# Kernel optimization log

Measured on AMD Instinct MI355X. Metric: run time of the kernel, lower is better.

Reference implementation:

```python
import jax, jax.numpy as jnp
import numpy as np

ATT_PROP = 2  # config['att_prop']
NEG_BIAS = 1e23


def _bucket(d):
    # standard coref-style distance bucketing into 10 buckets
    d = jnp.abs(d)
    return jnp.where(d <= 4, d,
           jnp.where(d <= 7, 5,
           jnp.where(d <= 15, 6,
           jnp.where(d <= 31, 7,
           jnp.where(d <= 63, 8, 9))))).astype(jnp.int32)


def setup_inputs() -> dict:
    key = jax.random.key(0)
    ks = jax.random.split(key, 12)
    B, N, M, D, H = 2, 1024, 2048, 512, 64
    scale = 0.02  # init_weights_std

    update = jax.random.normal(ks[0], (B, N, D), jnp.float32)
    span_begin = jnp.sort(jax.random.randint(ks[1], (B, N), 0, 2000), axis=-1).astype(jnp.int32)
    span_end = (span_begin + jax.random.randint(ks[2], (B, N), 0, 10)).astype(jnp.int32)
    square_mask = jnp.ones((B, N, N), jnp.float32)
    cand_span_vecs = jax.random.normal(ks[3], (B, M, D), jnp.float32)
    # unique prune indices per batch (a pruned span maps to one candidate slot)
    prune_indices_hoi = jnp.stack([
        jnp.sort(jax.random.permutation(jax.random.fold_in(ks[4], b), M)[:N])
        for b in range(B)]).astype(jnp.int32)
    span_lengths = jnp.array([900, 1024], dtype=jnp.int32)

    W_left = jax.random.normal(ks[5], (D, H), jnp.float32) * scale
    W_right = jax.random.normal(ks[6], (D, H), jnp.float32) * scale
    b_h = jnp.zeros((H,), jnp.float32)
    dist_emb = jax.random.normal(ks[7], (10, H), jnp.float32) * scale
    v_out = jax.random.normal(ks[8], (H,), jnp.float32) * scale
    b_out = jnp.zeros((), jnp.float32)
    W_gate = jax.random.normal(ks[9], (2 * D, D), jnp.float32) * scale
    b_gate = jnp.zeros((D,), jnp.float32)

    return dict(update=update, square_mask=square_mask, cand_span_vecs=cand_span_vecs,
                span_begin=span_begin, span_end=span_end,
                prune_indices_hoi=prune_indices_hoi, span_lengths=span_lengths,
                W_left=W_left, W_right=W_right, b_h=b_h, dist_emb=dist_emb,
                v_out=v_out, b_out=b_out, W_gate=W_gate, b_gate=b_gate)


def reference(update, square_mask, cand_span_vecs, span_begin, span_end,
              prune_indices_hoi, span_lengths, W_left, W_right, b_h,
              dist_emb, v_out, b_out, W_gate, b_gate):
    B, N, D = update.shape
    # pairwise distance features are iteration-invariant: precompute once
    dist = dist_emb[_bucket(span_begin[:, :, None] - span_begin[:, None, :])]  # [B,N,N,H]
    bias = -(1.0 - square_mask) * NEG_BIAS  # [B,N,N]

    for _ in range(ATT_PROP):
        left = update @ W_left    # [B,N,H]
        right = update @ W_right  # [B,N,H]
        h = jax.nn.relu(left[:, :, None, :] + right[:, None, :, :] + dist + b_h)  # [B,N,N,H]
        scores = jnp.einsum('bijh,h->bij', h, v_out) + b_out  # [B,N,N]
        probs = jax.nn.softmax(scores + bias, axis=-1)
        ctxt = jnp.einsum('bij,bjd->bid', probs, update)  # [B,N,D]
        g = jax.nn.sigmoid(jnp.concatenate([update, ctxt], axis=-1) @ W_gate + b_gate)
        update = g * update + (1.0 - g) * ctxt

    # overwrite_spans_hoi: scatter first span_lengths[b] updated vectors back
    valid = jnp.arange(N) < span_lengths[:, None]  # [B,N]

    def scatter_one(cand, idx, upd, m):
        cur = cand[idx]  # [N,D]
        vals = jnp.where(m[:, None], upd, cur)  # invalid rows write back original
        return cand.at[idx].set(vals)

    cand_new = jax.vmap(scatter_one)(cand_span_vecs, prune_indices_hoi, update, valid)
    return cand_new, update
```

## Files before the change

kernel.cpp:

```cpp
#include <hip/hip_runtime.h>
#include <cstdint>

#define NB 2
#define NN 1024
#define MM 2048
#define DD 512
#define HH 64
#define IT 16
#define JT 64
#define ST 68

typedef __attribute__((ext_vector_type(8))) short bf16x8;
typedef __attribute__((ext_vector_type(4))) float f32x4;

__device__ inline ushort f2bf(float x) {
  union { float f; uint32_t u; } v; v.f = x;
  uint32_t u = v.u;
  u += 0x7FFF + ((u >> 16) & 1);
  return (ushort)(u >> 16);
}

#define GLDS(gp, lp) \
  __builtin_amdgcn_global_load_lds( \
      (const __attribute__((address_space(1))) void*)(gp), \
      (__attribute__((address_space(3))) void*)(lp), 16, 0, 0)

__global__ __launch_bounds__(256) void lr_kernel(
    const float* __restrict__ U, const float* __restrict__ Wl,
    const float* __restrict__ Wr, float* __restrict__ left,
    float* __restrict__ right) {
  __shared__ float u[8][DD];
  const int block = blockIdx.x;
  const int tid = threadIdx.x;
  const float4* Uv = (const float4*)(U + (size_t)block * 8 * DD);
  float4* uv = (float4*)&u[0][0];
#pragma unroll
  for (int t = 0; t < 4; ++t) uv[tid + t * 256] = Uv[tid + t * 256];
  __syncthreads();
  const int h = tid & 63;
  const int isR = (tid >> 6) & 1;
  const int rbase = tid >> 7;
  const float* __restrict__ W = isR ? Wr : Wl;
  float acc[4] = {0.f, 0.f, 0.f, 0.f};
  for (int k0 = 0; k0 < DD; k0 += 4) {
    float w0 = W[(k0 + 0) * HH + h];
    float w1 = W[(k0 + 1) * HH + h];
    float w2 = W[(k0 + 2) * HH + h];
    float w3 = W[(k0 + 3) * HH + h];
#pragma unroll
    for (int r = 0; r < 4; ++r) {
      float4 u4 = *(const float4*)&u[rbase + r * 2][k0];
      acc[r] = fmaf(u4.w, w3, fmaf(u4.z, w2, fmaf(u4.y, w1, fmaf(u4.x, w0, acc[r]))));
    }
  }
  float* out = isR ? right : left;
#pragma unroll
  for (int r = 0; r < 4; ++r)
    out[(size_t)(block * 8 + rbase + r * 2) * HH + h] = acc[r];
}

__global__ __launch_bounds__(256) void conv_t(
    const float* __restrict__ in, ushort* __restrict__ out_row,
    ushort* __restrict__ out_T, int R, int C, int write_row) {
  __shared__ float tile[64][65];
  const int b = blockIdx.z;
  const int r0 = blockIdx.y * 64, c0 = blockIdx.x * 64;
  const int tx = threadIdx.x & 15, ty = threadIdx.x >> 4;
  const float* inb = in + (size_t)b * R * C;
#pragma unroll
  for (int p = 0; p < 4; ++p) {
    const int r = ty + p * 16;
    const float4 v = *(const float4*)&inb[(size_t)(r0 + r) * C + c0 + tx * 4];
    tile[r][tx * 4 + 0] = v.x; tile[r][tx * 4 + 1] = v.y;
    tile[r][tx * 4 + 2] = v.z; tile[r][tx * 4 + 3] = v.w;
    if (write_row) {
      ushort4 o = make_ushort4(f2bf(v.x), f2bf(v.y), f2bf(v.z), f2bf(v.w));
      *(ushort4*)&out_row[(size_t)b * R * C + (size_t)(r0 + r) * C + c0 + tx * 4] = o;
    }
  }
  __syncthreads();
  ushort* oT = out_T + (size_t)b * R * C;
#pragma unroll
  for (int p = 0; p < 4; ++p) {
    const int rr = ty + p * 16;
    ushort4 o;
    o.x = f2bf(tile[tx * 4 + 0][rr]);
    o.y = f2bf(tile[tx * 4 + 1][rr]);
    o.z = f2bf(tile[tx * 4 + 2][rr]);
    o.w = f2bf(tile[tx * 4 + 3][rr]);
    *(ushort4*)&oT[(size_t)(c0 + rr) * R + r0 + tx * 4] = o;
  }
}

__global__ __launch_bounds__(256) void score_compute(
    const float* __restrict__ left, const float* __restrict__ right,
    const int* __restrict__ span_begin, const float* __restrict__ mask,
    const float* __restrict__ dist_emb, const float* __restrict__ b_h,
    const float* __restrict__ v_out, float* __restrict__ scores) {
  __shared__ float Rt[JT][ST];
  __shared__ float LDb[IT * 10][ST];
  __shared__ float Lt[IT][ST];
  __shared__ float Dbh[10][ST];
  __shared__ float Vl[ST];
  __shared__ int sbi[IT];
  __shared__ int sbj[JT];
  const int b = blockIdx.z;
  const int i0 = blockIdx.y * IT;
  const int j0 = blockIdx.x * JT;
  const int tid = threadIdx.x;

  for (int f = tid; f < JT * 16; f += 256) {
    int r = f >> 4, h4 = f & 15;
    *(float4*)&Rt[r][h4 * 4] =
        *(const float4*)&right[((size_t)b * NN + j0 + r) * HH + h4 * 4];
  }
  {
    int r = tid >> 4, h4 = tid & 15;
    *(float4*)&Lt[r][h4 * 4] =
        *(const float4*)&left[((size_t)b * NN + i0 + r) * HH + h4 * 4];
  }
  for (int f = tid; f < 160; f += 256) {
    int bk = f >> 4, h4 = f & 15;
    float4 d = *(const float4*)&dist_emb[bk * HH + h4 * 4];
    float4 bh = *(const float4*)&b_h[h4 * 4];
    d.x += bh.x; d.y += bh.y; d.z += bh.z; d.w += bh.w;
    *(float4*)&Dbh[bk][h4 * 4] = d;
  }
  if (tid < 16) *(float4*)&Vl[tid * 4] = *(const float4*)&v_out[tid * 4];
  if (tid >= 64 && tid < 64 + IT) sbi[tid - 64] = span_begin[b * NN + i0 + tid - 64];
  if (tid >= 128 && tid < 128 + JT) sbj[tid - 128] = span_begin[b * NN + j0 + tid - 128];
  __syncthreads();
  {
    const int i = tid >> 4, h4 = tid & 15;
    const float4 l4 = *(const float4*)&Lt[i][h4 * 4];
#pragma unroll
    for (int bk = 0; bk < 10; ++bk) {
      float4 d = *(const float4*)&Dbh[bk][h4 * 4];
      d.x += l4.x; d.y += l4.y; d.z += l4.z; d.w += l4.w;
      *(float4*)&LDb[i * 10 + bk][h4 * 4] = d;
    }
  }
  __syncthreads();

  const int i = tid >> 4, jq = tid & 15;
  const float* LDbF = &LDb[0][0];
  const int my_sbi = sbi[i];
  int rowL[4];
#pragma unroll
  for (int jj = 0; jj < 4; ++jj) {
    const int jl = jq * 4 + jj;
    int d = sbj[jl] - my_sbi;
    d = d < 0 ? -d : d;
    const int bk =
        d <= 4 ? d : (d <= 7 ? 5 : (d <= 15 ? 6 : (d <= 31 ? 7 : (d <= 63 ? 8 : 9))));
    rowL[jj] = (i * 10 + bk) * ST;
  }
  float acc[4] = {0.f, 0.f, 0.f, 0.f};
#pragma unroll
  for (int hq = 0; hq < 16; ++hq) {
    const float4 v4 = *(const float4*)&Vl[hq * 4];
#pragma unroll
    for (int jj = 0; jj < 4; ++jj) {
      const float4 z = *(const float4*)&LDbF[rowL[jj] + hq * 4];
      const float4 r4 = *(const float4*)&Rt[jq * 4 + jj][hq * 4];
      float x0 = fmaxf(z.x + r4.x, 0.f);
      float x1 = fmaxf(z.y + r4.y, 0.f);
      float x2 = fmaxf(z.z + r4.z, 0.f);
      float x3 = fmaxf(z.w + r4.w, 0.f);
      acc[jj] = fmaf(x0, v4.x, acc[jj]);
      acc[jj] = fmaf(x1, v4.y, acc[jj]);
      acc[jj] = fmaf(x2, v4.z, acc[jj]);
      acc[jj] = fmaf(x3, v4.w, acc[jj]);
    }
  }
  const size_t rowoff = ((size_t)b * NN + i0 + i) * NN + j0 + jq * 4;
  const float4 m4 = *(const float4*)&mask[rowoff];
  float4 s4;
  s4.x = acc[0] - (1.0f - m4.x) * 1e23f;
  s4.y = acc[1] - (1.0f - m4.y) * 1e23f;
  s4.z = acc[2] - (1.0f - m4.z) * 1e23f;
  s4.w = acc[3] - (1.0f - m4.w) * 1e23f;
  *(float4*)&scores[rowoff] = s4;
}

__global__ __launch_bounds__(256) void softmax_bf(
    const float* __restrict__ scores, ushort* __restrict__ pbf) {
  const int wave = threadIdx.x >> 6, lane = threadIdx.x & 63;
  const int row = blockIdx.x * 4 + wave;
  const float4* p = (const float4*)(scores + (size_t)row * NN);
  float4 v[4];
  float mx = -3.0e38f;
#pragma unroll
  for (int q = 0; q < 4; ++q) {
    v[q] = p[lane + q * 64];
    mx = fmaxf(mx, fmaxf(fmaxf(v[q].x, v[q].y), fmaxf(v[q].z, v[q].w)));
  }
#pragma unroll
  for (int off = 32; off; off >>= 1) mx = fmaxf(mx, __shfl_xor(mx, off));
  float sum = 0.f;
#pragma unroll
  for (int q = 0; q < 4; ++q) {
    v[q].x = __expf(v[q].x - mx); v[q].y = __expf(v[q].y - mx);
    v[q].z = __expf(v[q].z - mx); v[q].w = __expf(v[q].w - mx);
    sum += v[q].x + v[q].y + v[q].z + v[q].w;
  }
#pragma unroll
  for (int off = 32; off; off >>= 1) sum += __shfl_xor(sum, off);
  const float inv = 1.0f / sum;
  ushort4* ob = (ushort4*)(pbf + (size_t)row * NN);
#pragma unroll
  for (int q = 0; q < 4; ++q) {
    ushort4 o = make_ushort4(f2bf(v[q].x * inv), f2bf(v[q].y * inv),
                             f2bf(v[q].z * inv), f2bf(v[q].w * inv));
    ob[lane + q * 64] = o;
  }
}

__global__ __launch_bounds__(256) void gemm_ctxt_mfma(
    const ushort* __restrict__ Pbf, const ushort* __restrict__ UT,
    float* __restrict__ Cf, ushort* __restrict__ Cbf) {
  __shared__ ushort As[64 * 64];
  __shared__ ushort Bs[64 * 64];
  const int b = blockIdx.z;
  const int m0 = blockIdx.y * 64, n0 = blockIdx.x * 64;
  const int tid = threadIdx.x;
  const int lane = tid & 63, wave = tid >> 6;
  const int wm = (wave >> 1) * 32, wn = (wave & 1) * 32;
  const ushort* Ab = Pbf + (size_t)b * NN * NN;
  const ushort* Bb = UT + (size_t)b * DD * NN;
  f32x4 acc[2][2] = {};
  const int fm = lane & 15, quad = lane >> 4;
  for (int k0 = 0; k0 < NN; k0 += 64) {
#pragma unroll
    for (int t = 0; t < 2; ++t) {
      const int idx = tid + t * 256;
      const int r = idx >> 3, c8 = idx & 7;
      const int g = c8 ^ (r & 7);
      GLDS(Ab + (size_t)(m0 + r) * NN + k0 + g * 8, As + idx * 8);
      GLDS(Bb + (size_t)(n0 + r) * NN + k0 + g * 8, Bs + idx * 8);
    }
    __syncthreads();
#pragma unroll
    for (int s = 0; s < 2; ++s) {
      bf16x8 af[2], bfr[2];
#pragma unroll
      for (int tm = 0; tm < 2; ++tm) {
        const int row = wm + tm * 16 + fm;
        const int c8 = (s * 4 + quad) ^ (row & 7);
        af[tm] = *(const bf16x8*)&As[row * 64 + c8 * 8];
      }
#pragma unroll
      for (int tn = 0; tn < 2; ++tn) {
        const int row = wn + tn * 16 + fm;
        const int c8 = (s * 4 + quad) ^ (row & 7);
        bfr[tn] = *(const bf16x8*)&Bs[row * 64 + c8 * 8];
      }
#pragma unroll
      for (int tm = 0; tm < 2; ++tm)
#pragma unroll
        for (int tn = 0; tn < 2; ++tn)
          acc[tm][tn] = __builtin_amdgcn_mfma_f32_16x16x32_bf16(
              af[tm], bfr[tn], acc[tm][tn], 0, 0, 0);
    }
    __syncthreads();
  }
#pragma unroll
  for (int tm = 0; tm < 2; ++tm)
#pragma unroll
    for (int tn = 0; tn < 2; ++tn) {
      const int col = n0 + wn + tn * 16 + fm;
#pragma unroll
      for (int r = 0; r < 4; ++r) {
        const int row = m0 + wm + tm * 16 + quad * 4 + r;
        const float vv = acc[tm][tn][r];
        const size_t off = (size_t)b * NN * DD + (size_t)row * DD + col;
        Cf[off] = vv;
        Cbf[off] = f2bf(vv);
      }
    }
}

__global__ __launch_bounds__(256) void gemm_gate_mfma(
    const ushort* __restrict__ Ubf, const ushort* __restrict__ Cbf,
    const ushort* __restrict__ WgT, const float* __restrict__ bg,
    const float* __restrict__ Uf, const float* __restrict__ Cf,
    float* __restrict__ Uout) {
  __shared__ ushort As[64 * 64];
  __shared__ ushort Bs[64 * 64];
  const int b = blockIdx.z;
  const int m0 = blockIdx.y * 64, n0 = blockIdx.x * 64;
  const int tid = threadIdx.x;
  const int lane = tid & 63, wave = tid >> 6;
  const int wm = (wave >> 1) * 32, wn = (wave & 1) * 32;
  f32x4 acc[2][2] = {};
  const int fm = lane & 15, quad = lane >> 4;
  for (int k0 = 0; k0 < 2 * DD; k0 += 64) {
    const ushort* Abase = (k0 < DD) ? (Ubf + (size_t)b * NN * DD)
                                    : (Cbf + (size_t)b * NN * DD);
    const int kc = k0 & (DD - 1);
#pragma unroll
    for (int t = 0; t < 2; ++t) {
      const int idx = tid + t * 256;
      const int r = idx >> 3, c8 = idx & 7;
      const int g = c8 ^ (r & 7);
      GLDS(Abase + (size_t)(m0 + r) * DD + kc + g * 8, As + idx * 8);
      GLDS(WgT + (size_t)(n0 + r) * (2 * DD) + k0 + g * 8, Bs + idx * 8);
    }
    __syncthreads();
#pragma unroll
    for (int s = 0; s < 2; ++s) {
      bf16x8 af[2], bfr[2];
#pragma unroll
      for (int tm = 0; tm < 2; ++tm) {
        const int row = wm + tm * 16 + fm;
        const int c8 = (s * 4 + quad) ^ (row & 7);
        af[tm] = *(const bf16x8*)&As[row * 64 + c8 * 8];
      }
#pragma unroll
      for (int tn = 0; tn < 2; ++tn) {
        const int row = wn + tn * 16 + fm;
        const int c8 = (s * 4 + quad) ^ (row & 7);
        bfr[tn] = *(const bf16x8*)&Bs[row * 64 + c8 * 8];
      }
#pragma unroll
      for (int tm = 0; tm < 2; ++tm)
#pragma unroll
        for (int tn = 0; tn < 2; ++tn)
          acc[tm][tn] = __builtin_amdgcn_mfma_f32_16x16x32_bf16(
              af[tm], bfr[tn], acc[tm][tn], 0, 0, 0);
    }
    __syncthreads();
  }
#pragma unroll
  for (int tm = 0; tm < 2; ++tm)
#pragma unroll
    for (int tn = 0; tn < 2; ++tn) {
      const int col = n0 + wn + tn * 16 + fm;
      const float bgv = bg[col];
#pragma unroll
      for (int r = 0; r < 4; ++r) {
        const int row = m0 + wm + tm * 16 + quad * 4 + r;
        const size_t off = (size_t)b * NN * DD + (size_t)row * DD + col;
        const float g = 1.f / (1.f + __expf(-(acc[tm][tn][r] + bgv)));
        Uout[off] = g * Uf[off] + (1.f - g) * Cf[off];
      }
    }
}

__global__ __launch_bounds__(256) void out_copy(
    const float* __restrict__ cand, const float* __restrict__ upd,
    float* __restrict__ out) {
  const int t = blockIdx.x * 256 + threadIdx.x;
  float4* o4 = (float4*)out;
  if (t < 524288) o4[t] = ((const float4*)cand)[t];
  else o4[t] = ((const float4*)upd)[t - 524288];
}

__global__ __launch_bounds__(128) void scatter_k(
    float* __restrict__ out_cand, const float* __restrict__ upd,
    const int* __restrict__ prune, const int* __restrict__ span_len) {
  const int row = blockIdx.x;
  const int b = row >> 10, i = row & 1023;
  if (i >= span_len[b]) return;
  const int dst = prune[row];
  const float4* src = (const float4*)(upd + (size_t)row * DD);
  float4* d = (float4*)(out_cand + ((size_t)b * MM + dst) * DD);
  d[threadIdx.x] = src[threadIdx.x];
}

extern "C" void kernel_launch(void* const* d_in, const int* in_sizes, int n_in,
                              void* d_out, int out_size, void* d_ws, size_t ws_size,
                              hipStream_t stream) {
  const float* update = (const float*)d_in[0];
  const float* mask = (const float*)d_in[1];
  const float* cand = (const float*)d_in[2];
  const int* span_begin = (const int*)d_in[3];
  const int* prune = (const int*)d_in[5];
  const int* span_len = (const int*)d_in[6];
  const float* Wl = (const float*)d_in[7];
  const float* Wr = (const float*)d_in[8];
  const float* b_h = (const float*)d_in[9];
  const float* dist_emb = (const float*)d_in[10];
  const float* v_out = (const float*)d_in[11];
  const float* Wg = (const float*)d_in[13];
  const float* b_gate = (const float*)d_in[14];

  char* w = (char*)d_ws;
  float* left = (float*)w;      w += (size_t)NB * NN * HH * 4;
  float* right = (float*)w;     w += (size_t)NB * NN * HH * 4;
  float* scores = (float*)w;    w += (size_t)NB * NN * NN * 4;
  ushort* probs_bf = (ushort*)w; w += (size_t)NB * NN * NN * 2;
  float* ctxt_f = (float*)w;    w += (size_t)NB * NN * DD * 4;
  ushort* ctxt_bf = (ushort*)w; w += (size_t)NB * NN * DD * 2;
  float* upd1 = (float*)w;      w += (size_t)NB * NN * DD * 4;
  float* upd2 = (float*)w;      w += (size_t)NB * NN * DD * 4;
  ushort* Ubf = (ushort*)w;     w += (size_t)NB * NN * DD * 2;
  ushort* UT = (ushort*)w;      w += (size_t)NB * NN * DD * 2;
  ushort* WgT = (ushort*)w;     w += (size_t)2 * DD * DD * 2;

  float* out = (float*)d_out;

  conv_t<<<dim3(8, 16, 1), 256, 0, stream>>>(Wg, WgT, WgT, 2 * DD, DD, 0);

  const float* Ucur = update;
  float* nexts[2] = {upd1, upd2};
  for (int it = 0; it < 2; ++it) {
    lr_kernel<<<256, 256, 0, stream>>>(Ucur, Wl, Wr, left, right);
    conv_t<<<dim3(8, 16, NB), 256, 0, stream>>>(Ucur, Ubf, UT, NN, DD, 1);
    score_compute<<<dim3(NN / JT, NN / IT, NB), 256, 0, stream>>>(
        left, right, span_begin, mask, dist_emb, b_h, v_out, scores);
    softmax_bf<<<NB * NN / 4, 256, 0, stream>>>(scores, probs_bf);
    gemm_ctxt_mfma<<<dim3(8, 16, NB), 256, 0, stream>>>(probs_bf, UT, ctxt_f, ctxt_bf);
    gemm_gate_mfma<<<dim3(8, 16, NB), 256, 0, stream>>>(Ubf, ctxt_bf, WgT, b_gate,
                                                        Ucur, ctxt_f, nexts[it]);
    Ucur = nexts[it];
  }
  out_copy<<<3072, 256, 0, stream>>>(cand, Ucur, out);
  scatter_k<<<NB * NN, 128, 0, stream>>>(out, Ucur, prune, span_len);
}
```

Before: 260.8 us.

## Fuse score computation with softmax and emit bf16 update copies from gate GEMM

```diff
diff --git a/kernel.cpp b/kernel.cpp
--- a/kernel.cpp
+++ b/kernel.cpp
@@ -6,8 +6,6 @@
 #define MM 2048
 #define DD 512
 #define HH 64
-#define IT 16
-#define JT 64
 #define ST 68
 
 typedef __attribute__((ext_vector_type(8))) short bf16x8;
@@ -92,33 +90,24 @@
   }
 }
 
-__global__ __launch_bounds__(256) void score_compute(
+__global__ __launch_bounds__(256) void score_softmax(
     const float* __restrict__ left, const float* __restrict__ right,
     const int* __restrict__ span_begin, const float* __restrict__ mask,
     const float* __restrict__ dist_emb, const float* __restrict__ b_h,
-    const float* __restrict__ v_out, float* __restrict__ scores) {
-  __shared__ float Rt[JT][ST];
-  __shared__ float LDb[IT * 10][ST];
-  __shared__ float Lt[IT][ST];
+    const float* __restrict__ v_out, ushort* __restrict__ probs_bf) {
+  __shared__ float Rt[64][ST];
+  __shared__ float LDb[4][10][ST];
   __shared__ float Dbh[10][ST];
+  __shared__ float Lt[4][ST];
   __shared__ float Vl[ST];
-  __shared__ int sbi[IT];
-  __shared__ int sbj[JT];
-  const int b = blockIdx.z;
-  const int i0 = blockIdx.y * IT;
-  const int j0 = blockIdx.x * JT;
+  __shared__ float Sc[4][NN];
+  __shared__ int sbj[NN];
+  const int b = blockIdx.y;
+  const int r0 = blockIdx.x * 4;
   const int tid = threadIdx.x;
-
-  for (int f = tid; f < JT * 16; f += 256) {
-    int r = f >> 4, h4 = f & 15;
-    *(float4*)&Rt[r][h4 * 4] =
-        *(const float4*)&right[((size_t)b * NN + j0 + r) * HH + h4 * 4];
-  }
-  {
-    int r = tid >> 4, h4 = tid & 15;
-    *(float4*)&Lt[r][h4 * 4] =
-        *(const float4*)&left[((size_t)b * NN + i0 + r) * HH + h4 * 4];
-  }
+  const int wave = tid >> 6, lane = tid & 63;
+  const int row = r0 + wave;
+
   for (int f = tid; f < 160; f += 256) {
     int bk = f >> 4, h4 = f & 15;
     float4 d = *(const float4*)&dist_emb[bk * HH + h4 * 4];
@@ -126,94 +115,82 @@
     d.x += bh.x; d.y += bh.y; d.z += bh.z; d.w += bh.w;
     *(float4*)&Dbh[bk][h4 * 4] = d;
   }
-  if (tid < 16) *(float4*)&Vl[tid * 4] = *(const float4*)&v_out[tid * 4];
-  if (tid >= 64 && tid < 64 + IT) sbi[tid - 64] = span_begin[b * NN + i0 + tid - 64];
-  if (tid >= 128 && tid < 128 + JT) sbj[tid - 128] = span_begin[b * NN + j0 + tid - 128];
+  if (tid < 64) {
+    int r = tid >> 4, h4 = tid & 15;
+    *(float4*)&Lt[r][h4 * 4] =
+        *(const float4*)&left[((size_t)b * NN + r0 + r) * HH + h4 * 4];
+  }
+  if (tid >= 64 && tid < 80)
+    *(float4*)&Vl[(tid - 64) * 4] = *(const float4*)&v_out[(tid - 64) * 4];
+  for (int t = tid; t < NN; t += 256) sbj[t] = span_begin[b * NN + t];
   __syncthreads();
-  {
-    const int i = tid >> 4, h4 = tid & 15;
-    const float4 l4 = *(const float4*)&Lt[i][h4 * 4];
-#pragma unroll
-    for (int bk = 0; bk < 10; ++bk) {
-      float4 d = *(const float4*)&Dbh[bk][h4 * 4];
-      d.x += l4.x; d.y += l4.y; d.z += l4.z; d.w += l4.w;
-      *(float4*)&LDb[i * 10 + bk][h4 * 4] = d;
-    }
-  }
-  __syncthreads();
-
-  const int i = tid >> 4, jq = tid & 15;
-  const float* LDbF = &LDb[0][0];
-  const int my_sbi = sbi[i];
-  int rowL[4];
-#pragma unroll
-  for (int jj = 0; jj < 4; ++jj) {
-    const int jl = jq * 4 + jj;
-    int d = sbj[jl] - my_sbi;
+  for (int f = tid; f < 640; f += 256) {
+    int i = f / 160, rem = f - i * 160;
+    int bk = rem >> 4, h4 = rem & 15;
+    float4 l = *(const float4*)&Lt[i][h4 * 4];
+    float4 d = *(const float4*)&Dbh[bk][h4 * 4];
+    d.x += l.x; d.y += l.y; d.z += l.z; d.w += l.w;
+    *(float4*)&LDb[i][bk][h4 * 4] = d;
+  }
+  float4 vr[16];
+#pragma unroll
+  for (int hq = 0; hq < 16; ++hq) vr[hq] = *(const float4*)&Vl[hq * 4];
+  const int my_sbi = span_begin[(size_t)b * NN + row];
+  const float* maskrow = mask + ((size_t)b * NN + row) * NN;
+
+#pragma unroll 1
+  for (int c = 0; c < 16; ++c) {
+    __syncthreads();
+#pragma unroll
+    for (int t = 0; t < 4; ++t) {
+      const int f = tid + t * 256;
+      const int r = f >> 4, h4 = f & 15;
+      *(float4*)&Rt[r][h4 * 4] =
+          *(const float4*)&right[((size_t)b * NN + c * 64 + r) * HH + h4 * 4];
+    }
+    __syncthreads();
+    int d = sbj[c * 64 + lane] - my_sbi;
     d = d < 0 ? -d : d;
     const int bk =
         d <= 4 ? d : (d <= 7 ? 5 : (d <= 15 ? 6 : (d <= 31 ? 7 : (d <= 63 ? 8 : 9))));
-    rowL[jj] = (i * 10 + bk) * ST;
-  }
-  float acc[4] = {0.f, 0.f, 0.f, 0.f};
-#pragma unroll
-  for (int hq = 0; hq < 16; ++hq) {
-    const float4 v4 = *(const float4*)&Vl[hq * 4];
-#pragma unroll
-    for (int jj = 0; jj < 4; ++jj) {
-      const float4 z = *(const float4*)&LDbF[rowL[jj] + hq * 4];
-      const float4 r4 = *(const float4*)&Rt[jq * 4 + jj][hq * 4];
+    const float* zp = &LDb[wave][bk][0];
+    const float* rp = &Rt[lane][0];
+    float acc = 0.f;
+#pragma unroll
+    for (int hq = 0; hq < 16; ++hq) {
+      const float4 z = *(const float4*)&zp[hq * 4];
+      const float4 r4 = *(const float4*)&rp[hq * 4];
       float x0 = fmaxf(z.x + r4.x, 0.f);
       float x1 = fmaxf(z.y + r4.y, 0.f);
       float x2 = fmaxf(z.z + r4.z, 0.f);
       float x3 = fmaxf(z.w + r4.w, 0.f);
-      acc[jj] = fmaf(x0, v4.x, acc[jj]);
-      acc[jj] = fmaf(x1, v4.y, acc[jj]);
-      acc[jj] = fmaf(x2, v4.z, acc[jj]);
-      acc[jj] = fmaf(x3, v4.w, acc[jj]);
-    }
-  }
-  const size_t rowoff = ((size_t)b * NN + i0 + i) * NN + j0 + jq * 4;
-  const float4 m4 = *(const float4*)&mask[rowoff];
-  float4 s4;
-  s4.x = acc[0] - (1.0f - m4.x) * 1e23f;
-  s4.y = acc[1] - (1.0f - m4.y) * 1e23f;
-  s4.z = acc[2] - (1.0f - m4.z) * 1e23f;
-  s4.w = acc[3] - (1.0f - m4.w) * 1e23f;
-  *(float4*)&scores[rowoff] = s4;
-}
-
-__global__ __launch_bounds__(256) void softmax_bf(
-    const float* __restrict__ scores, ushort* __restrict__ pbf) {
-  const int wave = threadIdx.x >> 6, lane = threadIdx.x & 63;
-  const int row = blockIdx.x * 4 + wave;
-  const float4* p = (const float4*)(scores + (size_t)row * NN);
-  float4 v[4];
+      acc = fmaf(x0, vr[hq].x, acc);
+      acc = fmaf(x1, vr[hq].y, acc);
+      acc = fmaf(x2, vr[hq].z, acc);
+      acc = fmaf(x3, vr[hq].w, acc);
+    }
+    const float mval = maskrow[c * 64 + lane];
+    Sc[wave][c * 64 + lane] = acc - (1.0f - mval) * 1e23f;
+  }
   float mx = -3.0e38f;
 #pragma unroll
-  for (int q = 0; q < 4; ++q) {
-    v[q] = p[lane + q * 64];
-    mx = fmaxf(mx, fmaxf(fmaxf(v[q].x, v[q].y), fmaxf(v[q].z, v[q].w)));
-  }
+  for (int c = 0; c < 16; ++c) mx = fmaxf(mx, Sc[wave][c * 64 + lane]);
 #pragma unroll
   for (int off = 32; off; off >>= 1) mx = fmaxf(mx, __shfl_xor(mx, off));
   float sum = 0.f;
 #pragma unroll
-  for (int q = 0; q < 4; ++q) {
-    v[q].x = __expf(v[q].x - mx); v[q].y = __expf(v[q].y - mx);
-    v[q].z = __expf(v[q].z - mx); v[q].w = __expf(v[q].w - mx);
-    sum += v[q].x + v[q].y + v[q].z + v[q].w;
+  for (int c = 0; c < 16; ++c) {
+    const float e = __expf(Sc[wave][c * 64 + lane] - mx);
+    Sc[wave][c * 64 + lane] = e;
+    sum += e;
   }
 #pragma unroll
   for (int off = 32; off; off >>= 1) sum += __shfl_xor(sum, off);
   const float inv = 1.0f / sum;
-  ushort4* ob = (ushort4*)(pbf + (size_t)row * NN);
-#pragma unroll
-  for (int q = 0; q < 4; ++q) {
-    ushort4 o = make_ushort4(f2bf(v[q].x * inv), f2bf(v[q].y * inv),
-                             f2bf(v[q].z * inv), f2bf(v[q].w * inv));
-    ob[lane + q * 64] = o;
-  }
+  ushort* prow = probs_bf + ((size_t)b * NN + row) * NN;
+#pragma unroll
+  for (int c = 0; c < 16; ++c)
+    prow[c * 64 + lane] = f2bf(Sc[wave][c * 64 + lane] * inv);
 }
 
 __global__ __launch_bounds__(256) void gemm_ctxt_mfma(
@@ -284,9 +261,11 @@
     const ushort* __restrict__ Ubf, const ushort* __restrict__ Cbf,
     const ushort* __restrict__ WgT, const float* __restrict__ bg,
     const float* __restrict__ Uf, const float* __restrict__ Cf,
-    float* __restrict__ Uout) {
+    float* __restrict__ Uout, ushort* __restrict__ UbfOut,
+    ushort* __restrict__ UTOut) {
   __shared__ ushort As[64 * 64];
   __shared__ ushort Bs[64 * 64];
+  __shared__ ushort Tt[64][66];
   const int b = blockIdx.z;
   const int m0 = blockIdx.y * 64, n0 = blockIdx.x * 64;
   const int tid = threadIdx.x;
@@ -335,16 +314,32 @@
   for (int tm = 0; tm < 2; ++tm)
 #pragma unroll
     for (int tn = 0; tn < 2; ++tn) {
-      const int col = n0 + wn + tn * 16 + fm;
+      const int cl = wn + tn * 16 + fm;
+      const int col = n0 + cl;
       const float bgv = bg[col];
 #pragma unroll
       for (int r = 0; r < 4; ++r) {
-        const int row = m0 + wm + tm * 16 + quad * 4 + r;
+        const int rl = wm + tm * 16 + quad * 4 + r;
+        const int row = m0 + rl;
         const size_t off = (size_t)b * NN * DD + (size_t)row * DD + col;
         const float g = 1.f / (1.f + __expf(-(acc[tm][tn][r] + bgv)));
-        Uout[off] = g * Uf[off] + (1.f - g) * Cf[off];
-      }
-    }
+        const float o = g * Uf[off] + (1.f - g) * Cf[off];
+        Uout[off] = o;
+        const ushort ob = f2bf(o);
+        UbfOut[off] = ob;
+        Tt[rl][cl] = ob;
+      }
+    }
+  __syncthreads();
+#pragma unroll
+  for (int p = 0; p < 4; ++p) {
+    const int cl = (tid >> 4) + p * 16;
+    const int rl = (tid & 15) * 4;
+    ushort4 o;
+    o.x = Tt[rl + 0][cl]; o.y = Tt[rl + 1][cl];
+    o.z = Tt[rl + 2][cl]; o.w = Tt[rl + 3][cl];
+    *(ushort4*)&UTOut[((size_t)b * DD + n0 + cl) * NN + m0 + rl] = o;
+  }
 }
 
 __global__ __launch_bounds__(256) void out_copy(
@@ -386,33 +381,34 @@
   const float* b_gate = (const float*)d_in[14];
 
   char* w = (char*)d_ws;
-  float* left = (float*)w;      w += (size_t)NB * NN * HH * 4;
-  float* right = (float*)w;     w += (size_t)NB * NN * HH * 4;
-  float* scores = (float*)w;    w += (size_t)NB * NN * NN * 4;
+  float* left = (float*)w;       w += (size_t)NB * NN * HH * 4;
+  float* right = (float*)w;      w += (size_t)NB * NN * HH * 4;
   ushort* probs_bf = (ushort*)w; w += (size_t)NB * NN * NN * 2;
-  float* ctxt_f = (float*)w;    w += (size_t)NB * NN * DD * 4;
-  ushort* ctxt_bf = (ushort*)w; w += (size_t)NB * NN * DD * 2;
-  float* upd1 = (float*)w;      w += (size_t)NB * NN * DD * 4;
-  float* upd2 = (float*)w;      w += (size_t)NB * NN * DD * 4;
-  ushort* Ubf = (ushort*)w;     w += (size_t)NB * NN * DD * 2;
-  ushort* UT = (ushort*)w;      w += (size_t)NB * NN * DD * 2;
-  ushort* WgT = (ushort*)w;     w += (size_t)2 * DD * DD * 2;
+  float* ctxt_f = (float*)w;     w += (size_t)NB * NN * DD * 4;
+  ushort* ctxt_bf = (ushort*)w;  w += (size_t)NB * NN * DD * 2;
+  float* upd1 = (float*)w;       w += (size_t)NB * NN * DD * 4;
+  float* upd2 = (float*)w;       w += (size_t)NB * NN * DD * 4;
+  ushort* Ubf0 = (ushort*)w;     w += (size_t)NB * NN * DD * 2;
+  ushort* Ubf1 = (ushort*)w;     w += (size_t)NB * NN * DD * 2;
+  ushort* UT = (ushort*)w;       w += (size_t)NB * NN * DD * 2;
+  ushort* WgT = (ushort*)w;      w += (size_t)2 * DD * DD * 2;
 
   float* out = (float*)d_out;
 
   conv_t<<<dim3(8, 16, 1), 256, 0, stream>>>(Wg, WgT, WgT, 2 * DD, DD, 0);
+  conv_t<<<dim3(8, 16, NB), 256, 0, stream>>>(update, Ubf0, UT, NN, DD, 1);
 
   const float* Ucur = update;
   float* nexts[2] = {upd1, upd2};
+  ushort* ubf_in[2] = {Ubf0, Ubf1};
+  ushort* ubf_out[2] = {Ubf1, Ubf0};
   for (int it = 0; it < 2; ++it) {
     lr_kernel<<<256, 256, 0, stream>>>(Ucur, Wl, Wr, left, right);
-    conv_t<<<dim3(8, 16, NB), 256, 0, stream>>>(Ucur, Ubf, UT, NN, DD, 1);
-    score_compute<<<dim3(NN / JT, NN / IT, NB), 256, 0, stream>>>(
-        left, right, span_begin, mask, dist_emb, b_h, v_out, scores);
-    softmax_bf<<<NB * NN / 4, 256, 0, stream>>>(scores, probs_bf);
+    score_softmax<<<dim3(NN / 4, NB), 256, 0, stream>>>(
+        left, right, span_begin, mask, dist_emb, b_h, v_out, probs_bf);
     gemm_ctxt_mfma<<<dim3(8, 16, NB), 256, 0, stream>>>(probs_bf, UT, ctxt_f, ctxt_bf);
-    gemm_gate_mfma<<<dim3(8, 16, NB), 256, 0, stream>>>(Ubf, ctxt_bf, WgT, b_gate,
-                                                        Ucur, ctxt_f, nexts[it]);
+    gemm_gate_mfma<<<dim3(8, 16, NB), 256, 0, stream>>>(
+        ubf_in[it], ctxt_bf, WgT, b_gate, Ucur, ctxt_f, nexts[it], ubf_out[it], UT);
     Ucur = nexts[it];
   }
   out_copy<<<3072, 256, 0, stream>>>(cand, Ucur, out);
```

New measurement: 241.1 us. 7.6% less time.
